# Kernel tuning notes

Hardware: AMD Instinct MI355X
Metric: run time of the kernel (lower is better)

The kernel has to match this reference:

```python
import jax, jax.numpy as jnp
import numpy as np

EMBED_DIM = 1024
NUM_HEADS = 16
HEAD_DIM = EMBED_DIM // NUM_HEADS


def setup_inputs() -> dict:
    key = jax.random.key(0)
    ks = jax.random.split(key, 11)
    B, S, D = 2, 2048, EMBED_DIM
    s = 1.0 / np.sqrt(D)
    inp = {
        "query": jax.random.normal(ks[0], (B, S, D), jnp.float32),
        "key": jax.random.normal(ks[1], (B, S, D), jnp.float32),
        "value": jax.random.normal(ks[2], (B, S, D), jnp.float32),
        # torch Linear weights: [out, in]
        "Wq": jax.random.normal(ks[3], (D, D), jnp.float32) * s,
        "bq": jnp.zeros((D,), jnp.float32),
        "Wk": jax.random.normal(ks[4], (D, D), jnp.float32) * s,
        "bk": jnp.zeros((D,), jnp.float32),
        "Wv": jax.random.normal(ks[5], (D, D), jnp.float32) * s,
        "bv": jnp.zeros((D,), jnp.float32),
        "Wo": jax.random.normal(ks[6], (D, D), jnp.float32) * s,
        "bo": jnp.zeros((D,), jnp.float32),
    }
    return inp


def reference(query, key, value, Wq, bq, Wk, bk, Wv, bv, Wo, bo):
    B, Q, D = query.shape
    K = key.shape[1]
    H, Hd = NUM_HEADS, HEAD_DIM
    # NOTE: source divides by scaling = head_dim**-0.5, i.e. multiplies by sqrt(head_dim)
    scaling = float(Hd) ** (-0.5)

    q = (query @ Wq.T + bq).reshape(B, Q, H, Hd).transpose(0, 2, 1, 3)  # [B,H,Q,Hd]
    k = (key @ Wk.T + bk).reshape(B, K, H, Hd).transpose(0, 2, 1, 3)    # [B,H,K,Hd]
    v = (value @ Wv.T + bv).reshape(B, K, H, Hd).transpose(0, 2, 1, 3)  # [B,H,K,Hd]

    scores = jnp.einsum("bhqd,bhkd->bhqk", q, k) / scaling
    attn = jax.nn.softmax(scores, axis=-1)  # dropout=0 (eval)
    out = jnp.einsum("bhqk,bhkd->bhqd", attn, v)
    out = out.transpose(0, 2, 1, 3).reshape(B, Q, D)
    return out @ Wo.T + bo
```

## Files before the change

kernel.cpp:

```cpp
#include <hip/hip_runtime.h>
#include <type_traits>
#include <utility>

#define B_ 2
#define S_ 2048
#define D_ 1024
#define H_ 16
#define HD_ 64
#define KDIM 1024

typedef __attribute__((ext_vector_type(8))) short    s16x8;
typedef __attribute__((ext_vector_type(8))) _Float16 h16x8;
typedef __attribute__((ext_vector_type(4))) float    f32x4;
typedef __attribute__((ext_vector_type(4))) int      i32x4;
typedef __attribute__((ext_vector_type(2))) int      i32x2;

template <typename T, typename = void> struct mfma_takes : std::false_type {};
template <typename T>
struct mfma_takes<T, std::void_t<decltype(__builtin_amdgcn_mfma_f32_16x16x32_f16(
    std::declval<T>(), std::declval<T>(), std::declval<f32x4>(), 0, 0, 0))>>
    : std::true_type {};
using frag8 = std::conditional_t<mfma_takes<h16x8>::value, h16x8, s16x8>;

__device__ __forceinline__ f32x4 mfma_f16(frag8 a, frag8 b, f32x4 c) {
  return __builtin_amdgcn_mfma_f32_16x16x32_f16(a, b, c, 0, 0, 0);
}

__device__ __forceinline__ short f2h(float f) {
  _Float16 h = (_Float16)f;
  short s; __builtin_memcpy(&s, &h, 2);
  return s;
}
__device__ __forceinline__ int pk2h(float a, float b) {
  auto p = __builtin_amdgcn_cvt_pkrtz(a, b);
  int r; __builtin_memcpy(&r, &p, 4); return r;
}
__device__ __forceinline__ frag8 ld_frag(const short* p) {
  return __builtin_bit_cast(frag8, *(const i32x4*)p);
}
__device__ __forceinline__ float fast_exp2(float x) {
  return __builtin_amdgcn_exp2f(x);
}

typedef __attribute__((address_space(1))) const void gvoid;
typedef __attribute__((address_space(3))) void lvoid;
__device__ __forceinline__ void async_copy16(const void* g, void* l) {
  __builtin_amdgcn_global_load_lds((gvoid*)g, (lvoid*)l, 16, 0, 0);
}

#define RAW_BARRIER() asm volatile("s_barrier" ::: "memory")
#define WAITCNT_VM(n) asm volatile("s_waitcnt vmcnt(" #n ")" ::: "memory")

__global__ __launch_bounds__(256)
void conv_all(const float* __restrict__ q, const float* __restrict__ k,
              const float* __restrict__ v, const float* __restrict__ Wq,
              const float* __restrict__ Wk, const float* __restrict__ Wv,
              const float* __restrict__ Wo,
              short* __restrict__ qh, short* __restrict__ kh,
              short* __restrict__ vh, short* __restrict__ wq,
              short* __restrict__ wk, short* __restrict__ wv,
              short* __restrict__ wo) {
  const int blk = blockIdx.x;
  const float* src; short* dst; int base;
  if (blk < 2048)      { src = q;  dst = qh; base = blk; }
  else if (blk < 4096) { src = k;  dst = kh; base = blk - 2048; }
  else if (blk < 6144) { src = v;  dst = vh; base = blk - 4096; }
  else if (blk < 6656) { src = Wq; dst = wq; base = blk - 6144; }
  else if (blk < 7168) { src = Wk; dst = wk; base = blk - 6656; }
  else if (blk < 7680) { src = Wv; dst = wv; base = blk - 7168; }
  else                 { src = Wo; dst = wo; base = blk - 7680; }
  const int i = base * 2048 + threadIdx.x * 8;
  float4 a0 = *(const float4*)(src + i);
  float4 a1 = *(const float4*)(src + i + 4);
  short h[8] = { f2h(a0.x), f2h(a0.y), f2h(a0.z), f2h(a0.w),
                 f2h(a1.x), f2h(a1.y), f2h(a1.z), f2h(a1.w) };
  i32x4 ph; __builtin_memcpy(&ph, h, 16);
  *(i32x4*)(dst + i) = ph;
}

__global__ __launch_bounds__(256, 3)
void gemm_qkv(const short* __restrict__ qh, const short* __restrict__ kh,
              const short* __restrict__ vh, const short* __restrict__ wq,
              const short* __restrict__ wk, const short* __restrict__ wv,
              const float* __restrict__ bq, const float* __restrict__ bk,
              const float* __restrict__ bv, short* __restrict__ Qf,
              short* __restrict__ Kf, short* __restrict__ Vt, float QS) {
  __shared__ short As[3 * 4096];
  __shared__ short Bs[3 * 4096];

  const int blk = blockIdx.x;
  const int xcd = blk & 7, i = blk >> 3;
  const int p = (i >> 3) * 8 + xcd;
  const int bn = i & 7;
  const int z = p >> 5, bm = p & 31;
  const short* Ap = z == 0 ? qh : z == 1 ? kh : vh;
  const short* Wp = z == 0 ? wq : z == 1 ? wk : wv;
  const float* bias = z == 0 ? bq : z == 1 ? bk : bv;
  short* Out = z == 0 ? Qf : z == 1 ? Kf : Vt;
  const float scale = z == 0 ? QS : 1.0f;
  const int omode = z == 2 ? 2 : 1;

  const int t = threadIdx.x, wave = t >> 6, lane = t & 63;
  const int laneN = lane & 15, quad = lane >> 4;
  const int wm = wave & 1, wn = wave >> 1;

  f32x4 acc[4][4];
#pragma unroll
  for (int i2 = 0; i2 < 4; ++i2)
#pragma unroll
    for (int j = 0; j < 4; ++j)
#pragma unroll
      for (int r = 0; r < 4; ++r) acc[i2][j][r] = 0.f;

  auto stage = [&](int buf, int kk) {
#pragma unroll
    for (int j = 0; j < 2; ++j) {
      const int chunk = j * 256 + t;
      const int row = chunk >> 2;
      const int gg = (chunk & 3) ^ ((row >> 1) & 3);
      async_copy16(Ap + (size_t)(bm * 128 + row) * KDIM + kk + gg * 8,
                   As + buf * 4096 + chunk * 8);
      async_copy16(Wp + (size_t)(bn * 128 + row) * KDIM + kk + gg * 8,
                   Bs + buf * 4096 + chunk * 8);
    }
  };

  stage(0, 0);
  stage(1, 32);
  int buf = 0;
  for (int kk = 0; kk < KDIM; kk += 32) {
    if (kk + 64 < KDIM) {
      int nb = buf + 2; if (nb >= 3) nb -= 3;
      stage(nb, kk + 64);
      WAITCNT_VM(8);
    } else if (kk + 32 < KDIM) {
      WAITCNT_VM(4);
    } else {
      WAITCNT_VM(0);
    }
    RAW_BARRIER();

    frag8 aF[4], bF[4];
#pragma unroll
    for (int mi = 0; mi < 4; ++mi) {
      const int row = wm * 64 + mi * 16 + laneN;
      aF[mi] = ld_frag(As + buf * 4096 + row * 32 +
                       ((quad ^ ((row >> 1) & 3)) * 8));
    }
#pragma unroll
    for (int ni = 0; ni < 4; ++ni) {
      const int row = wn * 64 + ni * 16 + laneN;
      bF[ni] = ld_frag(Bs + buf * 4096 + row * 32 +
                       ((quad ^ ((row >> 1) & 3)) * 8));
    }
#pragma unroll
    for (int mi = 0; mi < 4; ++mi)
#pragma unroll
      for (int ni = 0; ni < 4; ++ni)
        acc[mi][ni] = mfma_f16(aF[mi], bF[ni], acc[mi][ni]);
    RAW_BARRIER();
    buf = buf + 1 == 3 ? 0 : buf + 1;
  }

#pragma unroll
  for (int mi = 0; mi < 4; ++mi)
#pragma unroll
    for (int ni = 0; ni < 4; ++ni) {
      const int colg = bn * 128 + wn * 64 + ni * 16 + laneN;
      const float bb = bias[colg];
      if (omode == 2) {
        const int rowg0 = bm * 128 + wm * 64 + mi * 16 + quad * 4;
        const int b = rowg0 >> 11, s0 = rowg0 & 2047;
        const int h = colg >> 6, hd = colg & 63;
        short pk[4];
#pragma unroll
        for (int r = 0; r < 4; ++r) pk[r] = f2h(acc[mi][ni][r] + bb);
        i32x2 w; __builtin_memcpy(&w, pk, 8);
        *(i32x2*)(Vt + (((size_t)(b * H_ + h)) * HD_ + hd) * S_ + s0) = w;
      } else {
#pragma unroll
        for (int r = 0; r < 4; ++r) {
          const int rowg = bm * 128 + wm * 64 + mi * 16 + quad * 4 + r;
          const int b = rowg >> 11, s = rowg & 2047;
          const int h = colg >> 6, hd = colg & 63;
          Out[(((size_t)(b * H_ + h)) * S_ + s) * HD_ + hd] =
              f2h((acc[mi][ni][r] + bb) * scale);
        }
      }
    }
}

__global__ __launch_bounds__(256, 3)
void gemm_out(const short* __restrict__ Ap, const short* __restrict__ Wp,
              const float* __restrict__ bias, float* __restrict__ Out) {
  __shared__ short As[3 * 4096];
  __shared__ short Bs[3 * 2048];
  const int blk = blockIdx.x;
  const int xcd = blk & 7, i = blk >> 3;
  const int bm = (i >> 4) * 8 + xcd;
  const int bn = i & 15;

  const int t = threadIdx.x, wave = t >> 6, lane = t & 63;
  const int laneN = lane & 15, quad = lane >> 4;
  const int wm = wave & 1, wn = wave >> 1;

  f32x4 acc[4][2];
#pragma unroll
  for (int i2 = 0; i2 < 4; ++i2)
#pragma unroll
    for (int j = 0; j < 2; ++j)
#pragma unroll
      for (int r = 0; r < 4; ++r) acc[i2][j][r] = 0.f;

  auto stage = [&](int buf, int kk) {
#pragma unroll
    for (int j = 0; j < 2; ++j) {
      const int chunk = j * 256 + t;
      const int row = chunk >> 2;
      const int gg = (chunk & 3) ^ ((row >> 1) & 3);
      async_copy16(Ap + (size_t)(bm * 128 + row) * KDIM + kk + gg * 8,
                   As + buf * 4096 + chunk * 8);
    }
    {
      const int chunk = t;
      const int row = chunk >> 2;
      const int gg = (chunk & 3) ^ ((row >> 1) & 3);
      async_copy16(Wp + (size_t)(bn * 64 + row) * KDIM + kk + gg * 8,
                   Bs + buf * 2048 + chunk * 8);
    }
  };

  stage(0, 0);
  stage(1, 32);
  int buf = 0;
  for (int kk = 0; kk < KDIM; kk += 32) {
    if (kk + 64 < KDIM) {
      int nb = buf + 2; if (nb >= 3) nb -= 3;
      stage(nb, kk + 64);
      WAITCNT_VM(6);
    } else if (kk + 32 < KDIM) {
      WAITCNT_VM(3);
    } else {
      WAITCNT_VM(0);
    }
    RAW_BARRIER();

    frag8 aF[4], bF[2];
#pragma unroll
    for (int mi = 0; mi < 4; ++mi) {
      const int row = wm * 64 + mi * 16 + laneN;
      aF[mi] = ld_frag(As + buf * 4096 + row * 32 +
                       ((quad ^ ((row >> 1) & 3)) * 8));
    }
#pragma unroll
    for (int ni = 0; ni < 2; ++ni) {
      const int row = wn * 32 + ni * 16 + laneN;
      bF[ni] = ld_frag(Bs + buf * 2048 + row * 32 +
                       ((quad ^ ((row >> 1) & 3)) * 8));
    }
#pragma unroll
    for (int mi = 0; mi < 4; ++mi)
#pragma unroll
      for (int ni = 0; ni < 2; ++ni)
        acc[mi][ni] = mfma_f16(aF[mi], bF[ni], acc[mi][ni]);
    RAW_BARRIER();
    buf = buf + 1 == 3 ? 0 : buf + 1;
  }

#pragma unroll
  for (int mi = 0; mi < 4; ++mi)
#pragma unroll
    for (int ni = 0; ni < 2; ++ni) {
      const int colg = bn * 64 + wn * 32 + ni * 16 + laneN;
      const float bb = bias[colg];
#pragma unroll
      for (int r = 0; r < 4; ++r) {
        const int rowg = bm * 128 + wm * 64 + mi * 16 + quad * 4 + r;
        Out[(size_t)rowg * 1024 + colg] = acc[mi][ni][r] + bb;
      }
    }
}

__global__ __launch_bounds__(256, 4)
void attn(const short* __restrict__ Qf, const short* __restrict__ Kf,
          const short* __restrict__ Vt_, short* __restrict__ Ow) {
  __shared__ short Ks[2 * 4096];
  __shared__ short Vts[2 * 4096];
  __shared__ short Ps[4][16 * 64];

  const int blk = blockIdx.x;
  const int xcd = blk & 7, local = blk >> 3;
  const int pair = xcd * 4 + (local >> 5);
  const int h = pair & 15, b = pair >> 4, qt = local & 31;
  const size_t head = ((size_t)b * H_ + h) * (size_t)S_ * HD_;

  const int t = threadIdx.x;
  const int wave = t >> 6, lane = t & 63;
  const int laneN = lane & 15, quad = lane >> 4;

  frag8 qf[2];
  {
    const size_t row = (size_t)qt * 64 + wave * 16 + laneN;
#pragma unroll
    for (int half = 0; half < 2; ++half)
      qf[half] = ld_frag(Qf + head + row * HD_ + half * 32 + quad * 8);
  }

  f32x4 o[4];
  float m_r = -1e30f, l_r = 0.f;
#pragma unroll
  for (int i = 0; i < 4; ++i)
#pragma unroll
    for (int j = 0; j < 4; ++j) o[i][j] = 0.f;

  auto stage = [&](int buf, int kt) {
#pragma unroll
    for (int j = 0; j < 2; ++j) {
      const int chunk = j * 256 + t;
      const int row = chunk >> 3;
      const int g = (chunk & 7) ^ (row & 7);
      const int ldsoff = buf * 4096 + chunk * 8;
      async_copy16(Kf + head + (size_t)(kt * 64 + row) * HD_ + g * 8,
                   Ks + ldsoff);
      async_copy16(Vt_ + head + (size_t)row * S_ + kt * 64 + g * 8,
                   Vts + ldsoff);
    }
  };

  short* const pwr = &Ps[wave][0] + laneN * 64;
  const int rd0 = ((quad + laneN) & 7) * 8;
  const int rd1 = (((quad + 4) + laneN) & 7) * 8;

  stage(0, 0);
  int buf = 0;
  for (int kt = 0; kt < 32; ++kt, buf ^= 1) {
    if (kt + 1 < 32) {
      stage(buf ^ 1, kt + 1);
      WAITCNT_VM(4);
    } else {
      WAITCNT_VM(0);
    }
    RAW_BARRIER();

    const short* Kb = Ks + buf * 4096;
    const short* Vb = Vts + buf * 4096;

    frag8 vf[4][2];
#pragma unroll
    for (int dt = 0; dt < 4; ++dt) {
      const int row = dt * 16 + laneN;
#pragma unroll
      for (int half = 0; half < 2; ++half)
        vf[dt][half] = ld_frag(Vb + row * 64 +
                               (((half * 4 + quad) ^ (row & 7)) * 8));
    }

    f32x4 s[4];
#pragma unroll
    for (int nt = 0; nt < 4; ++nt) {
      const int row = nt * 16 + laneN;
      frag8 k0 = ld_frag(Kb + row * 64 + ((quad ^ (row & 7)) * 8));
      frag8 k1 = ld_frag(Kb + row * 64 + (((quad + 4) ^ (row & 7)) * 8));
      f32x4 acc;
#pragma unroll
      for (int j = 0; j < 4; ++j) acc[j] = 0.f;
      acc = mfma_f16(k0, qf[0], acc);
      acc = mfma_f16(k1, qf[1], acc);
      s[nt] = acc;
    }

    {
      float mt[4];
#pragma unroll
      for (int nt = 0; nt < 4; ++nt)
        mt[nt] = fmaxf(fmaxf(s[nt][0], s[nt][1]), fmaxf(s[nt][2], s[nt][3]));
      float mx = fmaxf(fmaxf(mt[0], mt[1]), fmaxf(mt[2], mt[3]));
      mx = fmaxf(mx, __shfl_xor(mx, 16));
      mx = fmaxf(mx, __shfl_xor(mx, 32));
      if (__any(mx > m_r + 8.f)) {
        const float mn = fmaxf(m_r, mx);
        const float al = fast_exp2(m_r - mn);
        m_r = mn;
        l_r *= al;
#pragma unroll
        for (int dt = 0; dt < 4; ++dt)
#pragma unroll
          for (int r = 0; r < 4; ++r) o[dt][r] *= al;
      }
      float rt[4];
#pragma unroll
      for (int nt = 0; nt < 4; ++nt) {
        const float p0 = fast_exp2(s[nt][0] - m_r);
        const float p1 = fast_exp2(s[nt][1] - m_r);
        const float p2 = fast_exp2(s[nt][2] - m_r);
        const float p3 = fast_exp2(s[nt][3] - m_r);
        s[nt][0] = p0; s[nt][1] = p1; s[nt][2] = p2; s[nt][3] = p3;
        rt[nt] = (p0 + p1) + (p2 + p3);
      }
      float rs = (rt[0] + rt[1]) + (rt[2] + rt[3]);
      rs += __shfl_xor(rs, 16);
      rs += __shfl_xor(rs, 32);
      l_r += rs;
    }

#pragma unroll
    for (int nt = 0; nt < 4; ++nt) {
      i32x2 w;
      w[0] = pk2h(s[nt][0], s[nt][1]);
      w[1] = pk2h(s[nt][2], s[nt][3]);
      const int g = nt * 2 + (quad >> 1);
      const int slot = (g + laneN) & 7;
      *(i32x2*)(pwr + slot * 8 + (quad & 1) * 4) = w;
    }
    const frag8 p0 = ld_frag(pwr + rd0);
    const frag8 p1 = ld_frag(pwr + rd1);
#pragma unroll
    for (int dt = 0; dt < 4; ++dt) {
      o[dt] = mfma_f16(vf[dt][0], p0, o[dt]);
      o[dt] = mfma_f16(vf[dt][1], p1, o[dt]);
    }
    RAW_BARRIER();
  }

  {
    const float inv = 1.0f / l_r;
    const int sg = qt * 64 + wave * 16 + laneN;
    short* dst = Ow + ((size_t)b * S_ + sg) * D_ + h * HD_;
#pragma unroll
    for (int dt = 0; dt < 4; ++dt) {
      short pk[4] = { f2h(o[dt][0] * inv), f2h(o[dt][1] * inv),
                      f2h(o[dt][2] * inv), f2h(o[dt][3] * inv) };
      i32x2 w; __builtin_memcpy(&w, pk, 8);
      *(i32x2*)(dst + dt * 16 + quad * 4) = w;
    }
  }
}

extern "C" void kernel_launch(void* const* d_in, const int* in_sizes, int n_in,
                              void* d_out, int out_size, void* d_ws, size_t ws_size,
                              hipStream_t stream) {
  const float* q  = (const float*)d_in[0];
  const float* k  = (const float*)d_in[1];
  const float* v  = (const float*)d_in[2];
  const float* Wq = (const float*)d_in[3];
  const float* bq = (const float*)d_in[4];
  const float* Wk = (const float*)d_in[5];
  const float* bk = (const float*)d_in[6];
  const float* Wv = (const float*)d_in[7];
  const float* bv = (const float*)d_in[8];
  const float* Wo = (const float*)d_in[9];
  const float* bo = (const float*)d_in[10];

  const size_t NTOK = (size_t)B_ * S_ * D_;
  const size_t NW   = (size_t)D_ * D_;
  short* p = (short*)d_ws;
  short* qh = p; p += NTOK;  short* kh = p; p += NTOK;  short* vh = p; p += NTOK;
  short* wq = p; p += NW;    short* wk = p; p += NW;
  short* wv = p; p += NW;    short* wo = p; p += NW;
  short* Qf = p; p += NTOK;  short* Kf = p; p += NTOK;
  short* Vt = p; p += NTOK;  short* Ow = p; p += NTOK;

  dim3 blk(256);

  conv_all<<<8192, blk, 0, stream>>>(q, k, v, Wq, Wk, Wv, Wo,
                                     qh, kh, vh, wq, wk, wv, wo);

  const float QS = 11.541560327111707f;
  gemm_qkv<<<768, blk, 0, stream>>>(qh, kh, vh, wq, wk, wv, bq, bk, bv,
                                    Qf, Kf, Vt, QS);

  attn<<<1024, dim3(256), 0, stream>>>(Qf, Kf, Vt, Ow);

  gemm_out<<<512, blk, 0, stream>>>(Ow, wo, bo, (float*)d_out);
}
```

Measured before the change: 233.2 us.

## Process two query sub-tiles per wave in attention to reuse K/V fragments

Each attention block now handles 128 query rows, with each wave owning two 16-row sub-tiles. K and V fragments are loaded from LDS once per key tile and reused for both sub-tiles, halving the K/V global staging and LDS reads per query row. Launch bounds drop from 4 to 2 blocks per CU to leave room for the doubled accumulator and fragment registers. The grid halves to 512 blocks, and staging pointers and LDS offsets are precomputed and incremented instead of recomputed each iteration. The cost is higher register pressure and lower occupancy, which may expose latency.

```diff
diff --git a/kernel.cpp b/kernel.cpp
--- a/kernel.cpp
+++ b/kernel.cpp
@@ -281,7 +281,7 @@
     }
 }
 
-__global__ __launch_bounds__(256, 4)
+__global__ __launch_bounds__(256, 2)
 void attn(const short* __restrict__ Qf, const short* __restrict__ Kf,
           const short* __restrict__ Vt_, short* __restrict__ Ow) {
   __shared__ short Ks[2 * 4096];
@@ -290,146 +290,161 @@
 
   const int blk = blockIdx.x;
   const int xcd = blk & 7, local = blk >> 3;
-  const int pair = xcd * 4 + (local >> 5);
-  const int h = pair & 15, b = pair >> 4, qt = local & 31;
+  const int pair = xcd * 4 + (local >> 4);
+  const int h = pair & 15, b = pair >> 4, qt = local & 15;
   const size_t head = ((size_t)b * H_ + h) * (size_t)S_ * HD_;
 
   const int t = threadIdx.x;
   const int wave = t >> 6, lane = t & 63;
   const int laneN = lane & 15, quad = lane >> 4;
 
-  frag8 qf[2];
-  {
-    const size_t row = (size_t)qt * 64 + wave * 16 + laneN;
+  frag8 qf[2][2];
+#pragma unroll
+  for (int sub = 0; sub < 2; ++sub) {
+    const size_t row = (size_t)qt * 128 + wave * 32 + sub * 16 + laneN;
 #pragma unroll
     for (int half = 0; half < 2; ++half)
-      qf[half] = ld_frag(Qf + head + row * HD_ + half * 32 + quad * 8);
-  }
-
-  f32x4 o[4];
-  float m_r = -1e30f, l_r = 0.f;
-#pragma unroll
-  for (int i = 0; i < 4; ++i)
-#pragma unroll
-    for (int j = 0; j < 4; ++j) o[i][j] = 0.f;
-
-  auto stage = [&](int buf, int kt) {
-#pragma unroll
-    for (int j = 0; j < 2; ++j) {
-      const int chunk = j * 256 + t;
-      const int row = chunk >> 3;
-      const int g = (chunk & 7) ^ (row & 7);
-      const int ldsoff = buf * 4096 + chunk * 8;
-      async_copy16(Kf + head + (size_t)(kt * 64 + row) * HD_ + g * 8,
-                   Ks + ldsoff);
-      async_copy16(Vt_ + head + (size_t)row * S_ + kt * 64 + g * 8,
-                   Vts + ldsoff);
-    }
-  };
+      qf[sub][half] = ld_frag(Qf + head + row * HD_ + half * 32 + quad * 8);
+  }
+
+  f32x4 o[2][4];
+  float m_r[2] = {-1e30f, -1e30f};
+  float l_r[2] = {0.f, 0.f};
+#pragma unroll
+  for (int sub = 0; sub < 2; ++sub)
+#pragma unroll
+    for (int i = 0; i < 4; ++i)
+#pragma unroll
+      for (int j = 0; j < 4; ++j) o[sub][i][j] = 0.f;
+
+  const int chunk0 = t, chunk1 = 256 + t;
+  const int row0 = chunk0 >> 3, g0 = (chunk0 & 7) ^ (row0 & 7);
+  const int row1 = chunk1 >> 3, g1 = (chunk1 & 7) ^ (row1 & 7);
+  const short* kp0 = Kf + head + (size_t)row0 * HD_ + g0 * 8;
+  const short* kp1 = Kf + head + (size_t)row1 * HD_ + g1 * 8;
+  const short* vp0 = Vt_ + head + (size_t)row0 * S_ + g0 * 8;
+  const short* vp1 = Vt_ + head + (size_t)row1 * S_ + g1 * 8;
+  const int d0 = chunk0 * 8, d1 = chunk1 * 8;
+
+  int off[4][2];
+#pragma unroll
+  for (int nt = 0; nt < 4; ++nt) {
+    const int row = nt * 16 + laneN;
+    off[nt][0] = row * 64 + ((quad ^ (row & 7)) * 8);
+    off[nt][1] = row * 64 + (((quad + 4) ^ (row & 7)) * 8);
+  }
 
   short* const pwr = &Ps[wave][0] + laneN * 64;
   const int rd0 = ((quad + laneN) & 7) * 8;
   const int rd1 = (((quad + 4) + laneN) & 7) * 8;
 
-  stage(0, 0);
+  {
+    async_copy16(kp0, Ks + d0);  async_copy16(kp1, Ks + d1);
+    async_copy16(vp0, Vts + d0); async_copy16(vp1, Vts + d1);
+    kp0 += 4096; kp1 += 4096; vp0 += 64; vp1 += 64;
+  }
   int buf = 0;
   for (int kt = 0; kt < 32; ++kt, buf ^= 1) {
     if (kt + 1 < 32) {
-      stage(buf ^ 1, kt + 1);
+      const int bo = buf ? 0 : 4096;
+      async_copy16(kp0, Ks + bo + d0);  async_copy16(kp1, Ks + bo + d1);
+      async_copy16(vp0, Vts + bo + d0); async_copy16(vp1, Vts + bo + d1);
+      kp0 += 4096; kp1 += 4096; vp0 += 64; vp1 += 64;
       WAITCNT_VM(4);
     } else {
       WAITCNT_VM(0);
     }
     RAW_BARRIER();
 
-    const short* Kb = Ks + buf * 4096;
-    const short* Vb = Vts + buf * 4096;
-
-    frag8 vf[4][2];
+    const short* Kb = Ks + (buf ? 4096 : 0);
+    const short* Vb = Vts + (buf ? 4096 : 0);
+
+    frag8 kf[4][2], vf[4][2];
+#pragma unroll
+    for (int nt = 0; nt < 4; ++nt) {
+#pragma unroll
+      for (int half = 0; half < 2; ++half) {
+        kf[nt][half] = ld_frag(Kb + off[nt][half]);
+        vf[nt][half] = ld_frag(Vb + off[nt][half]);
+      }
+    }
+
+#pragma unroll
+    for (int sub = 0; sub < 2; ++sub) {
+      f32x4 s[4];
+#pragma unroll
+      for (int nt = 0; nt < 4; ++nt) {
+        f32x4 acc;
+#pragma unroll
+        for (int j = 0; j < 4; ++j) acc[j] = 0.f;
+        acc = mfma_f16(kf[nt][0], qf[sub][0], acc);
+        acc = mfma_f16(kf[nt][1], qf[sub][1], acc);
+        s[nt] = acc;
+      }
+
+      {
+        float mt[4];
+#pragma unroll
+        for (int nt = 0; nt < 4; ++nt)
+          mt[nt] = fmaxf(fmaxf(s[nt][0], s[nt][1]), fmaxf(s[nt][2], s[nt][3]));
+        float mx = fmaxf(fmaxf(mt[0], mt[1]), fmaxf(mt[2], mt[3]));
+        mx = fmaxf(mx, __shfl_xor(mx, 16));
+        mx = fmaxf(mx, __shfl_xor(mx, 32));
+        if (__any(mx > m_r[sub] + 8.f)) {
+          const float mn = fmaxf(m_r[sub], mx);
+          const float al = fast_exp2(m_r[sub] - mn);
+          m_r[sub] = mn;
+          l_r[sub] *= al;
+#pragma unroll
+          for (int dt = 0; dt < 4; ++dt)
+#pragma unroll
+            for (int r = 0; r < 4; ++r) o[sub][dt][r] *= al;
+        }
+        float rt[4];
+#pragma unroll
+        for (int nt = 0; nt < 4; ++nt) {
+          const float p0 = fast_exp2(s[nt][0] - m_r[sub]);
+          const float p1 = fast_exp2(s[nt][1] - m_r[sub]);
+          const float p2 = fast_exp2(s[nt][2] - m_r[sub]);
+          const float p3 = fast_exp2(s[nt][3] - m_r[sub]);
+          s[nt][0] = p0; s[nt][1] = p1; s[nt][2] = p2; s[nt][3] = p3;
+          rt[nt] = (p0 + p1) + (p2 + p3);
+        }
+        float rs = (rt[0] + rt[1]) + (rt[2] + rt[3]);
+        rs += __shfl_xor(rs, 16);
+        rs += __shfl_xor(rs, 32);
+        l_r[sub] += rs;
+      }
+
+#pragma unroll
+      for (int nt = 0; nt < 4; ++nt) {
+        i32x2 w;
+        w[0] = pk2h(s[nt][0], s[nt][1]);
+        w[1] = pk2h(s[nt][2], s[nt][3]);
+        const int g = nt * 2 + (quad >> 1);
+        const int slot = (g + laneN) & 7;
+        *(i32x2*)(pwr + slot * 8 + (quad & 1) * 4) = w;
+      }
+      const frag8 p0 = ld_frag(pwr + rd0);
+      const frag8 p1 = ld_frag(pwr + rd1);
+#pragma unroll
+      for (int dt = 0; dt < 4; ++dt) {
+        o[sub][dt] = mfma_f16(vf[dt][0], p0, o[sub][dt]);
+        o[sub][dt] = mfma_f16(vf[dt][1], p1, o[sub][dt]);
+      }
+    }
+    RAW_BARRIER();
+  }
+
+#pragma unroll
+  for (int sub = 0; sub < 2; ++sub) {
+    const float inv = 1.0f / l_r[sub];
+    const int sg = qt * 128 + wave * 32 + sub * 16 + laneN;
+    short* dst = Ow + ((size_t)b * S_ + sg) * D_ + h * HD_;
 #pragma unroll
     for (int dt = 0; dt < 4; ++dt) {
-      const int row = dt * 16 + laneN;
-#pragma unroll
-      for (int half = 0; half < 2; ++half)
-        vf[dt][half] = ld_frag(Vb + row * 64 +
-                               (((half * 4 + quad) ^ (row & 7)) * 8));
-    }
-
-    f32x4 s[4];
-#pragma unroll
-    for (int nt = 0; nt < 4; ++nt) {
-      const int row = nt * 16 + laneN;
-      frag8 k0 = ld_frag(Kb + row * 64 + ((quad ^ (row & 7)) * 8));
-      frag8 k1 = ld_frag(Kb + row * 64 + (((quad + 4) ^ (row & 7)) * 8));
-      f32x4 acc;
-#pragma unroll
-      for (int j = 0; j < 4; ++j) acc[j] = 0.f;
-      acc = mfma_f16(k0, qf[0], acc);
-      acc = mfma_f16(k1, qf[1], acc);
-      s[nt] = acc;
-    }
-
-    {
-      float mt[4];
-#pragma unroll
-      for (int nt = 0; nt < 4; ++nt)
-        mt[nt] = fmaxf(fmaxf(s[nt][0], s[nt][1]), fmaxf(s[nt][2], s[nt][3]));
-      float mx = fmaxf(fmaxf(mt[0], mt[1]), fmaxf(mt[2], mt[3]));
-      mx = fmaxf(mx, __shfl_xor(mx, 16));
-      mx = fmaxf(mx, __shfl_xor(mx, 32));
-      if (__any(mx > m_r + 8.f)) {
-        const float mn = fmaxf(m_r, mx);
-        const float al = fast_exp2(m_r - mn);
-        m_r = mn;
-        l_r *= al;
-#pragma unroll
-        for (int dt = 0; dt < 4; ++dt)
-#pragma unroll
-          for (int r = 0; r < 4; ++r) o[dt][r] *= al;
-      }
-      float rt[4];
-#pragma unroll
-      for (int nt = 0; nt < 4; ++nt) {
-        const float p0 = fast_exp2(s[nt][0] - m_r);
-        const float p1 = fast_exp2(s[nt][1] - m_r);
-        const float p2 = fast_exp2(s[nt][2] - m_r);
-        const float p3 = fast_exp2(s[nt][3] - m_r);
-        s[nt][0] = p0; s[nt][1] = p1; s[nt][2] = p2; s[nt][3] = p3;
-        rt[nt] = (p0 + p1) + (p2 + p3);
-      }
-      float rs = (rt[0] + rt[1]) + (rt[2] + rt[3]);
-      rs += __shfl_xor(rs, 16);
-      rs += __shfl_xor(rs, 32);
-      l_r += rs;
-    }
-
-#pragma unroll
-    for (int nt = 0; nt < 4; ++nt) {
-      i32x2 w;
-      w[0] = pk2h(s[nt][0], s[nt][1]);
-      w[1] = pk2h(s[nt][2], s[nt][3]);
-      const int g = nt * 2 + (quad >> 1);
-      const int slot = (g + laneN) & 7;
-      *(i32x2*)(pwr + slot * 8 + (quad & 1) * 4) = w;
-    }
-    const frag8 p0 = ld_frag(pwr + rd0);
-    const frag8 p1 = ld_frag(pwr + rd1);
-#pragma unroll
-    for (int dt = 0; dt < 4; ++dt) {
-      o[dt] = mfma_f16(vf[dt][0], p0, o[dt]);
-      o[dt] = mfma_f16(vf[dt][1], p1, o[dt]);
-    }
-    RAW_BARRIER();
-  }
-
-  {
-    const float inv = 1.0f / l_r;
-    const int sg = qt * 64 + wave * 16 + laneN;
-    short* dst = Ow + ((size_t)b * S_ + sg) * D_ + h * HD_;
-#pragma unroll
-    for (int dt = 0; dt < 4; ++dt) {
-      short pk[4] = { f2h(o[dt][0] * inv), f2h(o[dt][1] * inv),
-                      f2h(o[dt][2] * inv), f2h(o[dt][3] * inv) };
+      short pk[4] = { f2h(o[sub][dt][0] * inv), f2h(o[sub][dt][1] * inv),
+                      f2h(o[sub][dt][2] * inv), f2h(o[sub][dt][3] * inv) };
       i32x2 w; __builtin_memcpy(&w, pk, 8);
       *(i32x2*)(dst + dt * 16 + quad * 4) = w;
     }
@@ -469,7 +484,7 @@
   gemm_qkv<<<768, blk, 0, stream>>>(qh, kh, vh, wq, wk, wv, bq, bk, bv,
                                     Qf, Kf, Vt, QS);
 
-  attn<<<1024, dim3(256), 0, stream>>>(Qf, Kf, Vt, Ow);
+  attn<<<512, dim3(256), 0, stream>>>(Qf, Kf, Vt, Ow);
 
   gemm_out<<<512, blk, 0, stream>>>(Ow, wo, bo, (float*)d_out);
 }
```

Result: no change. 235.0 us (+0.8%).

## Load K/V fragments directly from global memory in attention, drop LDS staging

Applied to the files above, without the earlier changes.

The attention kernel stops staging K and V tiles into shared memory with async copies and double buffering. Each wave now loads its MFMA fragments straight from global memory, relying on L2/cache reuse across waves. Blocks grow to 512 threads covering 128 query rows, with half as many blocks. This removes the per-tile barriers and LDS traffic, but risks higher global/cache load latency that is no longer hidden by prefetching, and each wave re-reads the same K/V data redundantly.

```diff
diff --git a/kernel.cpp b/kernel.cpp
--- a/kernel.cpp
+++ b/kernel.cpp
@@ -281,17 +281,15 @@
     }
 }
 
-__global__ __launch_bounds__(256, 4)
+__global__ __launch_bounds__(512, 4)
 void attn(const short* __restrict__ Qf, const short* __restrict__ Kf,
           const short* __restrict__ Vt_, short* __restrict__ Ow) {
-  __shared__ short Ks[2 * 4096];
-  __shared__ short Vts[2 * 4096];
-  __shared__ short Ps[4][16 * 64];
+  __shared__ short Ps[8][16 * 64];
 
   const int blk = blockIdx.x;
   const int xcd = blk & 7, local = blk >> 3;
-  const int pair = xcd * 4 + (local >> 5);
-  const int h = pair & 15, b = pair >> 4, qt = local & 31;
+  const int pair = xcd * 4 + (local >> 4);
+  const int h = pair & 15, b = pair >> 4, qt = local & 15;
   const size_t head = ((size_t)b * H_ + h) * (size_t)S_ * HD_;
 
   const int t = threadIdx.x;
@@ -300,7 +298,7 @@
 
   frag8 qf[2];
   {
-    const size_t row = (size_t)qt * 64 + wave * 16 + laneN;
+    const size_t row = (size_t)qt * 128 + wave * 16 + laneN;
 #pragma unroll
     for (int half = 0; half < 2; ++half)
       qf[half] = ld_frag(Qf + head + row * HD_ + half * 32 + quad * 8);
@@ -313,60 +311,44 @@
 #pragma unroll
     for (int j = 0; j < 4; ++j) o[i][j] = 0.f;
 
-  auto stage = [&](int buf, int kt) {
-#pragma unroll
-    for (int j = 0; j < 2; ++j) {
-      const int chunk = j * 256 + t;
-      const int row = chunk >> 3;
-      const int g = (chunk & 7) ^ (row & 7);
-      const int ldsoff = buf * 4096 + chunk * 8;
-      async_copy16(Kf + head + (size_t)(kt * 64 + row) * HD_ + g * 8,
-                   Ks + ldsoff);
-      async_copy16(Vt_ + head + (size_t)row * S_ + kt * 64 + g * 8,
-                   Vts + ldsoff);
-    }
-  };
+  int koff[4], voff[4];
+#pragma unroll
+  for (int nt = 0; nt < 4; ++nt) {
+    koff[nt] = (nt * 16 + laneN) * HD_ + quad * 8;
+    voff[nt] = (nt * 16 + laneN) * S_ + quad * 8;
+  }
 
   short* const pwr = &Ps[wave][0] + laneN * 64;
   const int rd0 = ((quad + laneN) & 7) * 8;
   const int rd1 = (((quad + 4) + laneN) & 7) * 8;
 
-  stage(0, 0);
-  int buf = 0;
-  for (int kt = 0; kt < 32; ++kt, buf ^= 1) {
-    if (kt + 1 < 32) {
-      stage(buf ^ 1, kt + 1);
-      WAITCNT_VM(4);
-    } else {
-      WAITCNT_VM(0);
-    }
-    RAW_BARRIER();
-
-    const short* Kb = Ks + buf * 4096;
-    const short* Vb = Vts + buf * 4096;
+  const short* Kt = Kf + head;
+  const short* Vp = Vt_ + head;
+
+  for (int kt = 0; kt < 32; ++kt, Kt += 64 * HD_, Vp += 64) {
+    frag8 kf[4][2];
+#pragma unroll
+    for (int nt = 0; nt < 4; ++nt) {
+      kf[nt][0] = ld_frag(Kt + koff[nt]);
+      kf[nt][1] = ld_frag(Kt + koff[nt] + 32);
+    }
+
+    f32x4 s[4];
+#pragma unroll
+    for (int nt = 0; nt < 4; ++nt) {
+      f32x4 acc;
+#pragma unroll
+      for (int j = 0; j < 4; ++j) acc[j] = 0.f;
+      acc = mfma_f16(kf[nt][0], qf[0], acc);
+      acc = mfma_f16(kf[nt][1], qf[1], acc);
+      s[nt] = acc;
+    }
 
     frag8 vf[4][2];
 #pragma unroll
     for (int dt = 0; dt < 4; ++dt) {
-      const int row = dt * 16 + laneN;
-#pragma unroll
-      for (int half = 0; half < 2; ++half)
-        vf[dt][half] = ld_frag(Vb + row * 64 +
-                               (((half * 4 + quad) ^ (row & 7)) * 8));
-    }
-
-    f32x4 s[4];
-#pragma unroll
-    for (int nt = 0; nt < 4; ++nt) {
-      const int row = nt * 16 + laneN;
-      frag8 k0 = ld_frag(Kb + row * 64 + ((quad ^ (row & 7)) * 8));
-      frag8 k1 = ld_frag(Kb + row * 64 + (((quad + 4) ^ (row & 7)) * 8));
-      f32x4 acc;
-#pragma unroll
-      for (int j = 0; j < 4; ++j) acc[j] = 0.f;
-      acc = mfma_f16(k0, qf[0], acc);
-      acc = mfma_f16(k1, qf[1], acc);
-      s[nt] = acc;
+      vf[dt][0] = ld_frag(Vp + voff[dt]);
+      vf[dt][1] = ld_frag(Vp + voff[dt] + 32);
     }
 
     {
@@ -419,12 +401,11 @@
       o[dt] = mfma_f16(vf[dt][0], p0, o[dt]);
       o[dt] = mfma_f16(vf[dt][1], p1, o[dt]);
     }
-    RAW_BARRIER();
   }
 
   {
     const float inv = 1.0f / l_r;
-    const int sg = qt * 64 + wave * 16 + laneN;
+    const int sg = qt * 128 + wave * 16 + laneN;
     short* dst = Ow + ((size_t)b * S_ + sg) * D_ + h * HD_;
 #pragma unroll
     for (int dt = 0; dt < 4; ++dt) {
@@ -469,7 +450,7 @@
   gemm_qkv<<<768, blk, 0, stream>>>(qh, kh, vh, wq, wk, wv, bq, bk, bv,
                                     Qf, Kf, Vt, QS);
 
-  attn<<<1024, dim3(256), 0, stream>>>(Qf, Kf, Vt, Ow);
+  attn<<<512, dim3(512), 0, stream>>>(Qf, Kf, Vt, Ow);
 
   gemm_out<<<512, blk, 0, stream>>>(Ow, wo, bo, (float*)d_out);
 }
```

Result: slower. 397.4 us (+70.4%).
